# Performance work log

Measured on AMD Instinct MI355X. Metric: run time of the kernel, lower is better.

The kernel has to match this reference:

```python
import jax, jax.numpy as jnp
import numpy as np

D = 64          # d_model
H = 128         # ffn_hidden_dim
N = 10000       # nodes
E = 50000       # edges
NEG_SLOPE = 0.01  # LeakyReLU default


def setup_inputs() -> dict:
    key = jax.random.key(0)
    ks = jax.random.split(key, 10)
    x = jax.random.normal(ks[0], (N, D), dtype=jnp.float32)
    edge_index = jax.random.randint(ks[1], (2, E), 0, N)
    edge_attr = jax.random.normal(ks[2], (E, D), dtype=jnp.float32)
    # MapE2NxN params (stored as [in, out] so forward is x @ W + b)
    w1 = jax.random.normal(ks[3], (D, H), dtype=jnp.float32) / np.sqrt(D)
    b1 = jnp.zeros((H,), dtype=jnp.float32)
    w2 = jax.random.normal(ks[4], (H, D * D), dtype=jnp.float32) / np.sqrt(H)
    b2 = jnp.zeros((D * D,), dtype=jnp.float32)
    # NNConv root weight + bias
    root = jax.random.normal(ks[5], (D, D), dtype=jnp.float32) / np.sqrt(D)
    bias = jnp.zeros((D,), dtype=jnp.float32)
    # LayerNorm affine params
    gamma = jnp.ones((D,), dtype=jnp.float32)
    beta = jnp.zeros((D,), dtype=jnp.float32)
    return {"x": x, "edge_attr": edge_attr, "gamma": gamma, "beta": beta,
            "w1": w1, "b1": b1, "w2": w2, "b2": b2,
            "root": root, "bias": bias, "edge_index": edge_index}


def _layer_norm(h, gamma, beta, eps=1e-5):
    mu = jnp.mean(h, axis=-1, keepdims=True)
    var = jnp.var(h, axis=-1, keepdims=True)
    return (h - mu) * jax.lax.rsqrt(var + eps) * gamma + beta


def _leaky_relu(h):
    return jnp.where(h >= 0, h, NEG_SLOPE * h)


def reference(x, edge_attr, gamma, beta, w1, b1, w2, b2, root, bias, edge_index):
    src, dst = edge_index[0], edge_index[1]
    # DeepGCNLayer block='res+': pre-activation norm -> act -> (dropout p=0) -> conv -> residual
    h = _leaky_relu(_layer_norm(x, gamma, beta))
    # MapE2NxN on edge attributes -> per-edge [D, D] weight matrix
    we = _leaky_relu(edge_attr @ w1 + b1) @ w2 + b2   # [E, D*D]
    we = we.reshape(E, D, D)
    # per-edge matvec with source node features (PyG NNConv message)
    msg = jnp.einsum('ed,edf->ef', h[src], we)        # [E, D]
    # scatter-mean aggregate into destination nodes
    agg = jax.ops.segment_sum(msg, dst, num_segments=N)
    cnt = jax.ops.segment_sum(jnp.ones((E,), dtype=msg.dtype), dst, num_segments=N)
    agg = agg / jnp.maximum(cnt, 1.0)[:, None]
    # root transform + bias, then residual
    out = agg + h @ root + bias
    return x + out
```

## Files before the change

### kernel.cpp

```cpp
#include <hip/hip_runtime.h>

#define NS 10000
#define DD 64
#define HH 128
#define EE 50000
#define SLOPE 0.01f

typedef __attribute__((ext_vector_type(8))) short short8;
typedef __attribute__((ext_vector_type(4))) float f32x4;

static __device__ __forceinline__ unsigned short f2bf(float f) {
  unsigned int u = __float_as_uint(f);
  u += 0x7fff + ((u >> 16) & 1);
  return (unsigned short)(u >> 16);
}

__device__ __forceinline__ float wave_sum64(float v) {
  #pragma unroll
  for (int m = 32; m >= 1; m >>= 1) v += __shfl_xor(v, m, 64);
  return v;
}

#define TBLK 128
__global__ __launch_bounds__(256) void k_prep(const float* __restrict__ x,
    const float* __restrict__ gamma, const float* __restrict__ beta,
    float* __restrict__ h, unsigned short* __restrict__ hbf,
    const float* __restrict__ ea, unsigned short* __restrict__ eabf,
    const float* __restrict__ w2, unsigned short* __restrict__ w2t2,
    const float* __restrict__ w1, unsigned short* __restrict__ w1t,
    const float* __restrict__ b2, unsigned short* __restrict__ b2t,
    const int* __restrict__ ei, int* __restrict__ cntsrc,
    int* __restrict__ cntdst) {
  __shared__ float tile[64][65];
  int t = threadIdx.x;
  int bid = blockIdx.x;
  if (bid < TBLK) {
    int k = bid;
    #pragma unroll
    for (int i = 0; i < 16; ++i) {
      int idx = t + i * 256;
      tile[idx >> 6][idx & 63] = w2[k * (DD * DD) + idx];
    }
    __syncthreads();
    #pragma unroll
    for (int it = 0; it < 2; ++it) {
      int slot = t + it * 256;
      int f = slot >> 3, l8 = slot & 7;
      short8 o;
      #pragma unroll
      for (int j = 0; j < 8; ++j) o[j] = f2bf(tile[l8 * 8 + j][f]);
      *(short8*)(w2t2 + ((size_t)(f * HH + k)) * DD + l8 * 8) = o;
    }
    return;
  }
  int pbid = bid - TBLK;
  int gid = pbid * 256 + t;
  if (gid < EE) {
    atomicAdd(&cntsrc[ei[gid]], 1);
    atomicAdd(&cntdst[ei[EE + gid]], 1);
  }
  if (gid < EE * DD / 8) {
    const float4* sp = (const float4*)(ea + (size_t)gid * 8);
    float4 v0 = sp[0], v1 = sp[1];
    short8 o;
    o[0] = f2bf(v0.x); o[1] = f2bf(v0.y); o[2] = f2bf(v0.z); o[3] = f2bf(v0.w);
    o[4] = f2bf(v1.x); o[5] = f2bf(v1.y); o[6] = f2bf(v1.z); o[7] = f2bf(v1.w);
    *(short8*)(eabf + (size_t)gid * 8) = o;
  }
  if (gid < DD * HH) {
    int d = gid & 63, hc = gid >> 6;
    w1t[gid] = f2bf(w1[d * HH + hc]);
  }
  if (gid < DD * DD) {
    int d = gid & 63, f = gid >> 6;
    b2t[gid] = f2bf(b2[d * DD + f]);
  }
  int wid = t >> 6;
  int lane = t & 63;
  int row = pbid * 4 + wid;
  if (row >= NS) return;
  float v = x[row * DD + lane];
  float s = wave_sum64(v);
  float s2 = wave_sum64(v * v);
  float mu = s * (1.0f / 64.0f);
  float var = s2 * (1.0f / 64.0f) - mu * mu;
  float r = rsqrtf(var + 1e-5f);
  float hn = (v - mu) * r * gamma[lane] + beta[lane];
  float hv = hn >= 0.f ? hn : SLOPE * hn;
  h[row * DD + lane] = hv;
  hbf[row * DD + lane] = f2bf(hv);
}

#define UBLK 782
#define CBLK 157
__global__ __launch_bounds__(256) void k_mid(
    const unsigned short* __restrict__ eabf, const unsigned short* __restrict__ w1t,
    const float* __restrict__ b1, unsigned short* __restrict__ ubf,
    const unsigned short* __restrict__ hbf, const unsigned short* __restrict__ b2t,
    float* __restrict__ cc, const int* __restrict__ cntsrc,
    int* __restrict__ rowptr, int* __restrict__ cursor) {
  int t = threadIdx.x;
  int bid = blockIdx.x;
  int w = t >> 6, lane = t & 63, lr = lane & 15, lg = lane >> 4;
  if (bid < UBLK) {
    int r0 = bid * 64 + w * 16;
    int ra = r0 + lr; if (ra >= EE) ra = EE - 1;
    short8 a0 = *(const short8*)(eabf + (size_t)ra * DD + lg * 8);
    short8 a1 = *(const short8*)(eabf + (size_t)ra * DD + 32 + lg * 8);
    short8 bb0[8], bb1[8];
    #pragma unroll
    for (int ni = 0; ni < 8; ++ni) {
      const unsigned short* bp = w1t + (ni * 16 + lr) * DD;
      bb0[ni] = *(const short8*)(bp + lg * 8);
      bb1[ni] = *(const short8*)(bp + 32 + lg * 8);
    }
    f32x4 acc[8] = {};
    #pragma unroll
    for (int ni = 0; ni < 8; ++ni) {
      acc[ni] = __builtin_amdgcn_mfma_f32_16x16x32_bf16(a0, bb0[ni], acc[ni], 0, 0, 0);
      acc[ni] = __builtin_amdgcn_mfma_f32_16x16x32_bf16(a1, bb1[ni], acc[ni], 0, 0, 0);
    }
    #pragma unroll
    for (int ni = 0; ni < 8; ++ni) {
      int col = ni * 16 + lr;
      float bb = b1[col];
      #pragma unroll
      for (int reg = 0; reg < 4; ++reg) {
        int gr = r0 + lg * 4 + reg;
        if (gr < EE) {
          float vv = acc[ni][reg] + bb;
          ubf[(size_t)gr * HH + col] = f2bf(vv >= 0.f ? vv : SLOPE * vv);
        }
      }
    }
  } else if (bid < UBLK + CBLK) {
    int row0 = (bid - UBLK) * 64;
    short8 a[4][2];
    #pragma unroll
    for (int mi = 0; mi < 4; ++mi) {
      int ra = row0 + mi * 16 + lr; if (ra >= NS) ra = NS - 1;
      a[mi][0] = *(const short8*)(hbf + (size_t)ra * DD + lg * 8);
      a[mi][1] = *(const short8*)(hbf + (size_t)ra * DD + 32 + lg * 8);
    }
    const unsigned short* bp = b2t + (w * 16 + lr) * DD;
    short8 b0 = *(const short8*)(bp + lg * 8);
    short8 b1v = *(const short8*)(bp + 32 + lg * 8);
    f32x4 acc[4] = {};
    #pragma unroll
    for (int mi = 0; mi < 4; ++mi) {
      acc[mi] = __builtin_amdgcn_mfma_f32_16x16x32_bf16(a[mi][0], b0, acc[mi], 0, 0, 0);
      acc[mi] = __builtin_amdgcn_mfma_f32_16x16x32_bf16(a[mi][1], b1v, acc[mi], 0, 0, 0);
    }
    #pragma unroll
    for (int mi = 0; mi < 4; ++mi)
      #pragma unroll
      for (int reg = 0; reg < 4; ++reg) {
        int gr = row0 + mi * 16 + lg * 4 + reg;
        if (gr < NS) cc[(size_t)gr * DD + w * 16 + lr] = acc[mi][reg];
      }
  } else {
    __shared__ int ps[256];
    const int CH = (NS + 255) / 256;
    int base = t * CH;
    int sum = 0;
    for (int i = 0; i < CH; ++i) {
      int idx = base + i;
      if (idx < NS) sum += cntsrc[idx];
    }
    ps[t] = sum;
    __syncthreads();
    for (int off = 1; off < 256; off <<= 1) {
      int v = (t >= off) ? ps[t - off] : 0;
      __syncthreads();
      ps[t] += v;
      __syncthreads();
    }
    int run = ps[t] - sum;
    for (int i = 0; i < CH; ++i) {
      int idx = base + i;
      if (idx < NS) {
        rowptr[idx] = run;
        cursor[idx] = run;
        run += cntsrc[idx];
      }
    }
    if (t == 255) rowptr[NS] = run;
  }
}

__global__ __launch_bounds__(256) void k_T_mfma(
    const unsigned short* __restrict__ hbf, const unsigned short* __restrict__ w2t2,
    unsigned short* __restrict__ T, int n0, int n1, int gx,
    const int* __restrict__ ei, int* __restrict__ cursor,
    int* __restrict__ eord, int doScatter) {
  __shared__ unsigned short As[64][72];
  __shared__ unsigned short Bs[128 * 72];
  int t = threadIdx.x;
  if (doScatter) {
    int gid = (blockIdx.y * gx + blockIdx.x) * 256 + t;
    if (gid < EE) {
      int s = ei[gid];
      int pos = atomicAdd(&cursor[s], 1);
      eord[pos] = gid;
    }
  }
  int row0 = n0 + blockIdx.x * 64;
  if (row0 >= n1) return;
  int col0 = blockIdx.y * 128;
  #pragma unroll
  for (int i = 0; i < 2; ++i) {
    int idx = t + i * 256;
    int r = idx >> 3, cc = (idx & 7) * 8;
    int gr = row0 + r;
    short8 v = {};
    if (gr < n1) v = *(const short8*)(hbf + (size_t)gr * DD + cc);
    *(short8*)(&As[r][cc]) = v;
  }
  #pragma unroll
  for (int i = 0; i < 4; ++i) {
    int idx = t + i * 256;
    int cL = idx >> 3, rr = (idx & 7) * 8;
    int gc = col0 + cL;
    short8 v = *(const short8*)(w2t2 + (size_t)gc * DD + rr);
    *(short8*)(&Bs[cL * 72 + rr]) = v;
  }
  __syncthreads();
  int w = t >> 6, lane = t & 63;
  int lr = lane & 15, lg = lane >> 4;
  f32x4 acc[4][2] = {};
  #pragma unroll
  for (int kk = 0; kk < 64; kk += 32) {
    short8 a[4], b[2];
    #pragma unroll
    for (int mi = 0; mi < 4; ++mi)
      a[mi] = *(const short8*)(&As[mi * 16 + lr][kk + lg * 8]);
    #pragma unroll
    for (int ni = 0; ni < 2; ++ni)
      b[ni] = *(const short8*)(&Bs[(w * 32 + ni * 16 + lr) * 72 + kk + lg * 8]);
    #pragma unroll
    for (int mi = 0; mi < 4; ++mi)
      #pragma unroll
      for (int ni = 0; ni < 2; ++ni)
        acc[mi][ni] = __builtin_amdgcn_mfma_f32_16x16x32_bf16(
            a[mi], b[ni], acc[mi][ni], 0, 0, 0);
  }
  __syncthreads();
  #pragma unroll
  for (int mi = 0; mi < 4; ++mi)
    #pragma unroll
    for (int ni = 0; ni < 2; ++ni) {
      int col = w * 32 + ni * 16 + lr;
      #pragma unroll
      for (int reg = 0; reg < 4; ++reg)
        Bs[(mi * 16 + lg * 4 + reg) * 132 + col] = f2bf(acc[mi][ni][reg]);
    }
  __syncthreads();
  #pragma unroll
  for (int i = 0; i < 4; ++i) {
    int idx = t + i * 256;
    int row = idx >> 4, seg = idx & 15;
    int gr = row0 + row;
    if (gr < n1) {
      short8 v = *(const short8*)(&Bs[row * 132 + seg * 8]);
      *(short8*)(T + (size_t)(gr - n0) * (HH * DD) + col0 + seg * 8) = v;
    }
  }
}

__global__ __launch_bounds__(256) void k_msg_wave(
    const unsigned short* __restrict__ ubf, const unsigned short* __restrict__ T,
    const float* __restrict__ cc, const int* __restrict__ ei,
    const int* __restrict__ rowptr, const int* __restrict__ eord,
    float* __restrict__ agg, int n0, int n1) {
  int wid = threadIdx.x >> 6;
  int lane = threadIdx.x & 63;
  int s = n0 + blockIdx.x * 64 + blockIdx.y * 4 + wid;
  if (s >= n1) return;
  int beg = rowptr[s];
  int deg = rowptr[s + 1] - beg;
  if (deg == 0) return;
  int lr = lane & 15, lg = lane >> 4;
  int ev = 0, dv = 0;
  if (lane < 16 && lane < deg) {
    ev = eord[beg + lane];
    dv = ei[EE + ev];
  }
  const unsigned short* tp = T + (size_t)(s - n0) * (HH * DD);
  short8 b[4][4];
  #pragma unroll
  for (int ft = 0; ft < 4; ++ft)
    #pragma unroll
    for (int kk = 0; kk < 4; ++kk)
      b[ft][kk] =
          *(const short8*)(tp + (ft * 16 + lr) * HH + kk * 32 + lg * 8);
  float clv[4];
  #pragma unroll
  for (int ft = 0; ft < 4; ++ft) clv[ft] = cc[(size_t)s * DD + ft * 16 + lr];

  for (int p0 = 0; p0 < deg; p0 += 16) {
    if (p0) {
      ev = 0; dv = 0;
      if (lane < 16 && p0 + lane < deg) {
        ev = eord[beg + p0 + lane];
        dv = ei[EE + ev];
      }
    }
    int el = __shfl(ev, (p0 + lr < deg) ? lr : 0);
    const unsigned short* up = ubf + (size_t)el * HH;
    short8 au[4];
    #pragma unroll
    for (int kk = 0; kk < 4; ++kk)
      au[kk] = *(const short8*)(up + kk * 32 + lg * 8);
    f32x4 acc[4] = {};
    #pragma unroll
    for (int kk = 0; kk < 4; ++kk)
      #pragma unroll
      for (int ft = 0; ft < 4; ++ft)
        acc[ft] = __builtin_amdgcn_mfma_f32_16x16x32_bf16(au[kk], b[ft][kk],
                                                          acc[ft], 0, 0, 0);
    #pragma unroll
    for (int reg = 0; reg < 4; ++reg) {
      int eidx = p0 + lg * 4 + reg;
      int dstn = __shfl(dv, lg * 4 + reg);
      if (eidx < deg) {
        #pragma unroll
        for (int ft = 0; ft < 4; ++ft)
          atomicAdd(&agg[(size_t)dstn * DD + ft * 16 + lr],
                    acc[ft][reg] + clv[ft]);
      }
    }
  }
}

__global__ __launch_bounds__(256) void k_final(const float* __restrict__ x,
    const float* __restrict__ h, const float* __restrict__ root,
    const float* __restrict__ bias, const float* __restrict__ agg,
    const int* __restrict__ cnt, float* __restrict__ out) {
  __shared__ float Bs[DD][DD + 1];
  __shared__ float As[32][DD];
  int t = threadIdx.x;
  #pragma unroll
  for (int i = 0; i < 16; ++i) {
    int idx = t + i * 256;
    Bs[idx >> 6][idx & 63] = root[idx];
  }
  int row0 = blockIdx.x * 32;
  #pragma unroll
  for (int i = 0; i < 8; ++i) {
    int idx = t + i * 256;
    int r = idx >> 6, d = idx & 63;
    int gr = row0 + r;
    As[r][d] = (gr < NS) ? h[gr * DD + d] : 0.f;
  }
  __syncthreads();
  int r = t >> 3;
  int c0 = (t & 7) * 8;
  int gr = row0 + r;
  if (gr >= NS) return;
  float acc[8] = {};
  for (int d = 0; d < DD; ++d) {
    float a = As[r][d];
    #pragma unroll
    for (int j = 0; j < 8; ++j) acc[j] += a * Bs[d][c0 + j];
  }
  float inv = 1.0f / fmaxf((float)cnt[gr], 1.0f);
  #pragma unroll
  for (int j = 0; j < 8; ++j) {
    size_t gi = (size_t)gr * DD + c0 + j;
    out[gi] = x[gi] + agg[gi] * inv + acc[j] + bias[c0 + j];
  }
}

extern "C" void kernel_launch(void* const* d_in, const int* in_sizes, int n_in,
                              void* d_out, int out_size, void* d_ws, size_t ws_size,
                              hipStream_t stream) {
  const float* x     = (const float*)d_in[0];
  const float* ea    = (const float*)d_in[1];
  const float* gamma = (const float*)d_in[2];
  const float* beta  = (const float*)d_in[3];
  const float* w1    = (const float*)d_in[4];
  const float* b1    = (const float*)d_in[5];
  const float* w2    = (const float*)d_in[6];
  const float* b2    = (const float*)d_in[7];
  const float* root  = (const float*)d_in[8];
  const float* bias  = (const float*)d_in[9];
  const int*   ei    = (const int*)d_in[10];
  float* out = (float*)d_out;

  char* p = (char*)d_ws;
  auto carve = [&](size_t bytes) {
    char* q = p;
    p += (bytes + 255) & ~(size_t)255;
    return q;
  };
  float* h             = (float*)carve(sizeof(float) * NS * DD);
  unsigned short* hbf  = (unsigned short*)carve(sizeof(short) * NS * DD);
  float* cc            = (float*)carve(sizeof(float) * NS * DD);
  unsigned short* w2t2 = (unsigned short*)carve(sizeof(short) * HH * DD * DD);
  unsigned short* w1t  = (unsigned short*)carve(sizeof(short) * DD * HH);
  unsigned short* b2t  = (unsigned short*)carve(sizeof(short) * DD * DD);
  unsigned short* eabf = (unsigned short*)carve(sizeof(short) * (size_t)EE * DD);
  unsigned short* ubf  = (unsigned short*)carve(sizeof(short) * (size_t)EE * HH);
  int* rowptr          = (int*)carve(sizeof(int) * (NS + 1));
  int* cursor          = (int*)carve(sizeof(int) * NS);
  int* eord            = (int*)carve(sizeof(int) * EE);
  char* z0 = p;
  float* agg           = (float*)carve(sizeof(float) * NS * DD);
  int* cntdst          = (int*)carve(sizeof(int) * NS);
  int* cntsrc          = (int*)carve(sizeof(int) * NS);
  size_t zlen = (size_t)(p - z0);
  size_t fixed = (size_t)(p - (char*)d_ws);

  size_t freeb = (ws_size > fixed) ? (ws_size - fixed - 256) : 0;
  int rows = (int)(freeb / (sizeof(short) * HH * DD));
  if (rows >= NS) rows = NS;
  else { rows &= ~63; if (rows < 64) rows = 64; }
  unsigned short* Tt = (unsigned short*)carve(sizeof(short) * (size_t)rows * HH * DD);

  hipMemsetAsync(z0, 0, zlen, stream);
  k_prep<<<dim3(TBLK + (NS + 3) / 4), dim3(256), 0, stream>>>(
      x, gamma, beta, h, hbf, ea, eabf, w2, w2t2, w1, w1t, b2, b2t,
      ei, cntsrc, cntdst);
  k_mid<<<dim3(UBLK + CBLK + 1), dim3(256), 0, stream>>>(
      eabf, w1t, b1, ubf, hbf, b2t, cc, cntsrc, rowptr, cursor);

  for (int n0 = 0; n0 < NS; n0 += rows) {
    int n1 = n0 + rows;
    if (n1 > NS) n1 = NS;
    int nr = n1 - n0;
    int gx = (((nr + 63) / 64) + 7) & ~7;
    k_T_mfma<<<dim3(gx, (HH * DD) / 128), dim3(256), 0, stream>>>(
        hbf, w2t2, Tt, n0, n1, gx, ei, cursor, eord, n0 == 0 ? 1 : 0);
    k_msg_wave<<<dim3(gx, 16), dim3(256), 0, stream>>>(
        ubf, Tt, cc, ei, rowptr, eord, agg, n0, n1);
  }

  k_final<<<dim3((NS + 31) / 32), dim3(256), 0, stream>>>(x, h, root, bias, agg,
                                                          cntdst, out);
}
```

Before: 136.1 us.

## Fuse edge-MLP/prefix-scan kernel with T-GEMM launch and split out scatter

```diff
diff --git a/kernel.cpp b/kernel.cpp
--- a/kernel.cpp
+++ b/kernel.cpp
@@ -93,16 +93,22 @@
 
 #define UBLK 782
 #define CBLK 157
-__global__ __launch_bounds__(256) void k_mid(
+#define TSTART 944
+__global__ __launch_bounds__(256) void k_midT(
     const unsigned short* __restrict__ eabf, const unsigned short* __restrict__ w1t,
     const float* __restrict__ b1, unsigned short* __restrict__ ubf,
     const unsigned short* __restrict__ hbf, const unsigned short* __restrict__ b2t,
     float* __restrict__ cc, const int* __restrict__ cntsrc,
-    int* __restrict__ rowptr, int* __restrict__ cursor) {
+    int* __restrict__ rowptr, int* __restrict__ cursor,
+    const unsigned short* __restrict__ w2t2, unsigned short* __restrict__ T,
+    int n0, int n1, int gx, int doMid) {
+  __shared__ unsigned short As[64][72];
+  __shared__ unsigned short Bs[128 * 72];
   int t = threadIdx.x;
   int bid = blockIdx.x;
   int w = t >> 6, lane = t & 63, lr = lane & 15, lg = lane >> 4;
   if (bid < UBLK) {
+    if (!doMid) return;
     int r0 = bid * 64 + w * 16;
     int ra = r0 + lr; if (ra >= EE) ra = EE - 1;
     short8 a0 = *(const short8*)(eabf + (size_t)ra * DD + lg * 8);
@@ -133,7 +139,9 @@
         }
       }
     }
+    return;
   } else if (bid < UBLK + CBLK) {
+    if (!doMid) return;
     int row0 = (bid - UBLK) * 64;
     short8 a[4][2];
     #pragma unroll
@@ -158,8 +166,10 @@
         int gr = row0 + mi * 16 + lg * 4 + reg;
         if (gr < NS) cc[(size_t)gr * DD + w * 16 + lr] = acc[mi][reg];
       }
-  } else {
-    __shared__ int ps[256];
+    return;
+  } else if (bid == UBLK + CBLK) {
+    if (!doMid) return;
+    int* ps = (int*)&As[0][0];
     const int CH = (NS + 255) / 256;
     int base = t * CH;
     int sum = 0;
@@ -185,36 +195,22 @@
       }
     }
     if (t == 255) rowptr[NS] = run;
-  }
-}
-
-__global__ __launch_bounds__(256) void k_T_mfma(
-    const unsigned short* __restrict__ hbf, const unsigned short* __restrict__ w2t2,
-    unsigned short* __restrict__ T, int n0, int n1, int gx,
-    const int* __restrict__ ei, int* __restrict__ cursor,
-    int* __restrict__ eord, int doScatter) {
-  __shared__ unsigned short As[64][72];
-  __shared__ unsigned short Bs[128 * 72];
-  int t = threadIdx.x;
-  if (doScatter) {
-    int gid = (blockIdx.y * gx + blockIdx.x) * 256 + t;
-    if (gid < EE) {
-      int s = ei[gid];
-      int pos = atomicAdd(&cursor[s], 1);
-      eord[pos] = gid;
-    }
-  }
-  int row0 = n0 + blockIdx.x * 64;
+    return;
+  }
+  if (bid < TSTART) return;
+  int tb = bid - TSTART;
+  int bx = tb % gx, by = tb / gx;
+  int row0 = n0 + bx * 64;
   if (row0 >= n1) return;
-  int col0 = blockIdx.y * 128;
+  int col0 = by * 128;
   #pragma unroll
   for (int i = 0; i < 2; ++i) {
     int idx = t + i * 256;
-    int r = idx >> 3, cc = (idx & 7) * 8;
+    int r = idx >> 3, cc2 = (idx & 7) * 8;
     int gr = row0 + r;
     short8 v = {};
-    if (gr < n1) v = *(const short8*)(hbf + (size_t)gr * DD + cc);
-    *(short8*)(&As[r][cc]) = v;
+    if (gr < n1) v = *(const short8*)(hbf + (size_t)gr * DD + cc2);
+    *(short8*)(&As[r][cc2]) = v;
   }
   #pragma unroll
   for (int i = 0; i < 4; ++i) {
@@ -225,8 +221,6 @@
     *(short8*)(&Bs[cL * 72 + rr]) = v;
   }
   __syncthreads();
-  int w = t >> 6, lane = t & 63;
-  int lr = lane & 15, lg = lane >> 4;
   f32x4 acc[4][2] = {};
   #pragma unroll
   for (int kk = 0; kk < 64; kk += 32) {
@@ -264,6 +258,16 @@
       short8 v = *(const short8*)(&Bs[row * 132 + seg * 8]);
       *(short8*)(T + (size_t)(gr - n0) * (HH * DD) + col0 + seg * 8) = v;
     }
+  }
+}
+
+__global__ __launch_bounds__(256) void k_scatter(const int* __restrict__ ei,
+    int* __restrict__ cursor, int* __restrict__ eord) {
+  int e = blockIdx.x * 256 + threadIdx.x;
+  if (e < EE) {
+    int s = ei[e];
+    int pos = atomicAdd(&cursor[s], 1);
+    eord[pos] = e;
   }
 }
 
@@ -421,18 +425,21 @@
   k_prep<<<dim3(TBLK + (NS + 3) / 4), dim3(256), 0, stream>>>(
       x, gamma, beta, h, hbf, ea, eabf, w2, w2t2, w1, w1t, b2, b2t,
       ei, cntsrc, cntdst);
-  k_mid<<<dim3(UBLK + CBLK + 1), dim3(256), 0, stream>>>(
-      eabf, w1t, b1, ubf, hbf, b2t, cc, cntsrc, rowptr, cursor);
-
+
+  bool first = true;
   for (int n0 = 0; n0 < NS; n0 += rows) {
     int n1 = n0 + rows;
     if (n1 > NS) n1 = NS;
     int nr = n1 - n0;
     int gx = (((nr + 63) / 64) + 7) & ~7;
-    k_T_mfma<<<dim3(gx, (HH * DD) / 128), dim3(256), 0, stream>>>(
-        hbf, w2t2, Tt, n0, n1, gx, ei, cursor, eord, n0 == 0 ? 1 : 0);
+    k_midT<<<dim3(TSTART + gx * (HH * DD / 128)), dim3(256), 0, stream>>>(
+        eabf, w1t, b1, ubf, hbf, b2t, cc, cntsrc, rowptr, cursor,
+        w2t2, Tt, n0, n1, gx, first ? 1 : 0);
+    if (first)
+      k_scatter<<<dim3((EE + 255) / 256), dim3(256), 0, stream>>>(ei, cursor, eord);
     k_msg_wave<<<dim3(gx, 16), dim3(256), 0, stream>>>(
         ubf, Tt, cc, ei, rowptr, eord, agg, n0, n1);
+    first = false;
   }
 
   k_final<<<dim3((NS + 31) / 32), dim3(256), 0, stream>>>(x, h, root, bias, agg,
```

New measurement: 119.5 us. 1.14x faster.
